# Performance work log

Measured on AMD Instinct MI355X. Metric: run time of the kernel, lower is better.

The kernel has to match this reference:

```python
import jax, jax.numpy as jnp
import numpy as np

EPS = 1e-5

def _layernorm(x, w, b):
    mu = jnp.mean(x, axis=-1, keepdims=True)
    var = jnp.mean(jnp.square(x - mu), axis=-1, keepdims=True)
    return (x - mu) * jax.lax.rsqrt(var + EPS) * w + b

def setup_inputs() -> dict:
    key = jax.random.key(0)
    ks = jax.random.split(key, 9)
    N, P_DIM, D = 16384, 3072, 1024
    patches = jax.random.normal(ks[0], (N, P_DIM), dtype=jnp.float32)
    bbox_coords = jax.random.uniform(ks[1], (N, 4), dtype=jnp.float32)
    ln1_w = jnp.ones((P_DIM,), dtype=jnp.float32)
    ln1_b = jnp.zeros((P_DIM,), dtype=jnp.float32)
    W_patch = jax.random.normal(ks[2], (D, P_DIM), dtype=jnp.float32) * (P_DIM ** -0.5)
    class_emb = jax.random.normal(ks[3], (1, 1, D), dtype=jnp.float32)
    W_pos = jax.random.normal(ks[4], (D, 4), dtype=jnp.float32) * 0.5
    b_pos = jax.random.normal(ks[5], (D,), dtype=jnp.float32) * 0.02
    class_pos = jax.random.normal(ks[6], (1, D), dtype=jnp.float32)
    return {"patches": patches, "bbox_coords": bbox_coords, "ln1_w": ln1_w,
            "ln1_b": ln1_b, "W_patch": W_patch, "class_emb": class_emb,
            "W_pos": W_pos, "b_pos": b_pos, "class_pos": class_pos}

def reference(patches, bbox_coords, ln1_w, ln1_b, W_patch, class_emb, W_pos, b_pos, class_pos):
    # Batched equivalent of the per-patch loop: LayerNorm -> Linear (no bias).
    # NOTE: torch code computes patch_norm2 but appends the PRE-norm2 embedding,
    # so norm2 is dead code and omitted here.
    x = _layernorm(patches, ln1_w, ln1_b)                      # [N, patch_dim]
    patch_embeds = jnp.einsum('np,dp->nd', x, W_patch)          # [N, D]
    embeddings = jnp.concatenate([class_emb, patch_embeds[None]], axis=1)  # [1, N+1, D]
    pos = jnp.einsum('nc,dc->nd', bbox_coords, W_pos) + b_pos   # [N, D]
    pos_full = jnp.concatenate([class_pos[None], pos[None]], axis=1)       # [1, N+1, D]
    return embeddings + pos_full
```

## Files before the change

### kernel.cpp

```cpp
#include <hip/hip_runtime.h>

typedef unsigned short u16;
typedef __attribute__((ext_vector_type(8))) short bf16x8;
typedef __attribute__((ext_vector_type(16))) float f32x16;

#define AS1C(p) ((const __attribute__((address_space(1))) void*)(p))
#define AS3(p)  ((__attribute__((address_space(3))) void*)(p))

#define CFENCE() asm volatile("" ::: "memory")

__device__ __forceinline__ u16 f2bf(float f) {
    unsigned u = __float_as_uint(f);
    u += 0x7fffu + ((u >> 16) & 1u);
    return (u16)(u >> 16);
}

__global__ __launch_bounds__(256) void prep_kernel(
    const float* __restrict__ x, const float* __restrict__ w,
    const float* __restrict__ b, const float* __restrict__ Wp,
    const float* __restrict__ ce, const float* __restrict__ cp,
    u16* __restrict__ A, u16* __restrict__ Wb, float* __restrict__ out,
    int N, int D, int K)
{
    const int blk = blockIdx.x;
    const int t = threadIdx.x;

    if (blk < N) {
        const float* xr = x + (size_t)blk * K;
        float4 v[3];
#pragma unroll
        for (int i = 0; i < 3; ++i)
            v[i] = *(const float4*)&xr[(i * 256 + t) * 4];

        float s = 0.f;
#pragma unroll
        for (int i = 0; i < 3; ++i) s += v[i].x + v[i].y + v[i].z + v[i].w;
#pragma unroll
        for (int off = 32; off; off >>= 1) s += __shfl_down(s, off);

        __shared__ float red[8];
        const int wid = t >> 6, lane = t & 63;
        if (lane == 0) red[wid] = s;
        __syncthreads();
        const float mu = (red[0] + red[1] + red[2] + red[3]) * (1.0f / 3072.0f);

        float sq = 0.f;
#pragma unroll
        for (int i = 0; i < 3; ++i) {
            float dx = v[i].x - mu, dy = v[i].y - mu, dz = v[i].z - mu, dw = v[i].w - mu;
            sq += dx * dx + dy * dy + dz * dz + dw * dw;
        }
#pragma unroll
        for (int off = 32; off; off >>= 1) sq += __shfl_down(sq, off);
        if (lane == 0) red[4 + wid] = sq;
        __syncthreads();
        const float var = (red[4] + red[5] + red[6] + red[7]) * (1.0f / 3072.0f);
        const float inv = rsqrtf(var + 1e-5f);

#pragma unroll
        for (int i = 0; i < 3; ++i) {
            const int j = (i * 256 + t) * 4;
            const float4 wv = *(const float4*)&w[j];
            const float4 bv = *(const float4*)&b[j];
            ushort4 o;
            o.x = f2bf((v[i].x - mu) * inv * wv.x + bv.x);
            o.y = f2bf((v[i].y - mu) * inv * wv.y + bv.y);
            o.z = f2bf((v[i].z - mu) * inv * wv.z + bv.z);
            o.w = f2bf((v[i].w - mu) * inv * wv.w + bv.w);
            *(ushort4*)&A[(size_t)blk * K + j] = o;
        }
    } else if (blk < N + D) {
        const int row = blk - N;
        const float* wr = Wp + (size_t)row * K;
#pragma unroll
        for (int i = 0; i < 3; ++i) {
            const int j = (i * 256 + t) * 4;
            const float4 v = *(const float4*)&wr[j];
            ushort4 o;
            o.x = f2bf(v.x); o.y = f2bf(v.y); o.z = f2bf(v.z); o.w = f2bf(v.w);
            *(ushort4*)&Wb[(size_t)row * K + j] = o;
        }
    } else {
#pragma unroll
        for (int i = 0; i < 4; ++i) {
            const int j = i * 256 + t;
            out[j] = ce[j] + cp[j];
        }
    }
}

#define STG_A(BUFOFS, R0, T_) \
    __builtin_amdgcn_global_load_lds(AS1C(aS + (size_t)(R0) * 3072 + (T_) * 64), \
                                     AS3(dA + (BUFOFS) + (R0) * 128), 16, 0, 0)
#define STG_B(BUFOFS, R0, T_) \
    __builtin_amdgcn_global_load_lds(AS1C(bS + (size_t)(R0) * 3072 + (T_) * 64), \
                                     AS3(dB + (BUFOFS) + (R0) * 128), 16, 0, 0)

#define MFMA32(d, a, b) d = __builtin_amdgcn_mfma_f32_32x32x16_bf16(a, b, d, 0, 0, 0)

#define LGKM(N_) asm volatile("s_waitcnt lgkmcnt(" #N_ ")" ::: "memory"); \
                 __builtin_amdgcn_sched_barrier(0)

#define PH32(BUF, CK, STG, WT) do {                                               \
    const char* Ab = L + (BUF) + aRowBase;                                        \
    const char* Bb = L + (BUF) + bRowBase;                                        \
    bf16x8 a0 = *(const bf16x8*)(Ab + 0 * 4096 + (CK));                           \
    bf16x8 a1 = *(const bf16x8*)(Ab + 1 * 4096 + (CK));                           \
    bf16x8 b0 = *(const bf16x8*)(Bb + 0 * 4096 + (CK));                           \
    bf16x8 b1 = *(const bf16x8*)(Bb + 1 * 4096 + (CK));                           \
    bf16x8 a2 = *(const bf16x8*)(Ab + 2 * 4096 + (CK));                           \
    bf16x8 a3 = *(const bf16x8*)(Ab + 3 * 4096 + (CK));                           \
    STG;                                                                          \
    __builtin_amdgcn_s_setprio(1);                                                \
    LGKM(2);                                                                      \
    MFMA32(acc[0][0], a0, b0); MFMA32(acc[1][0], a1, b0);                         \
    MFMA32(acc[0][1], a0, b1); MFMA32(acc[1][1], a1, b1);                         \
    LGKM(0);                                                                      \
    MFMA32(acc[2][0], a2, b0); MFMA32(acc[3][0], a3, b0);                         \
    MFMA32(acc[2][1], a2, b1); MFMA32(acc[3][1], a3, b1);                         \
    __builtin_amdgcn_s_setprio(0);                                                \
    WT;                                                                           \
    __builtin_amdgcn_s_barrier();                                                 \
    CFENCE();                                                                     \
} while (0)

__global__ __launch_bounds__(512, 2) void gemm_256_r13_kernel(
    const u16* __restrict__ A, const u16* __restrict__ W,
    const float* __restrict__ bbox, const float* __restrict__ Wpos,
    const float* __restrict__ bpos, float* __restrict__ out,
    int D)
{
    __shared__ __align__(16) char lds[131072];
    const char* L = (const char*)lds;
    const int K = 3072;
    const int NK = 48;

    const int bid = blockIdx.x;
    const int swb = (bid & 7) * 32 + (bid >> 3);
    const int bx = swb & 3;
    const int by = swb >> 2;
    const int brow = by * 256;
    const int bcol = bx * 256;

    const int t = threadIdx.x;
    const int wid = t >> 6, lane = t & 63;
    const int wm = wid >> 2;
    const int wn = wid & 3;
    const int l31 = lane & 31;
    const int klane16 = (lane >> 5) * 16;
    const int xorb = (lane & 7) << 4;
    const int aRowBase = (wm * 128 + l31) * 128;
    const int bRowBase = 32768 + (wn * 64 + l31) * 128;
    const int ck0 = (0  + klane16) ^ xorb;
    const int ck1 = (32 + klane16) ^ xorb;
    const int ck2 = (64 + klane16) ^ xorb;
    const int ck3 = (96 + klane16) ^ xorb;

    const int srow = t >> 3;
    const int scol = ((t & 7) ^ ((t >> 3) & 7)) * 8;
    const u16* aS = A + (size_t)(brow + srow) * K + scol;
    const u16* bS = W + (size_t)(bcol + srow) * K + scol;
    char* dA = (char*)lds + t * 16;
    char* dB = (char*)lds + 32768 + t * 16;

    f32x16 acc[4][2] = {};

    STG_B(0, 0, 0);   STG_B(0, 64, 0);  STG_B(0, 128, 0); STG_B(0, 192, 0);
    STG_A(0, 0, 0);   STG_A(0, 128, 0); STG_A(0, 64, 0);  STG_A(0, 192, 0);
    asm volatile("s_waitcnt vmcnt(0)" ::: "memory");
    __builtin_amdgcn_s_barrier();
    CFENCE();

    for (int T = 0; T < NK; T += 2) {
        const bool more = (T + 2) < NK;
        PH32(0, ck0, { STG_B(65536, 0, T + 1); STG_B(65536, 64, T + 1);
                       STG_B(65536, 128, T + 1); }, ((void)0));
        PH32(0, ck1, { STG_B(65536, 192, T + 1); STG_A(65536, 0, T + 1);
                       STG_A(65536, 128, T + 1); }, ((void)0));
        PH32(0, ck2, { STG_A(65536, 64, T + 1); STG_A(65536, 192, T + 1); }, ((void)0));
        PH32(0, ck3, ((void)0),
             { asm volatile("s_waitcnt vmcnt(0)" ::: "memory"); });
        PH32(65536, ck0, { if (more) { STG_B(0, 0, T + 2); STG_B(0, 64, T + 2);
                                       STG_B(0, 128, T + 2); } }, ((void)0));
        PH32(65536, ck1, { if (more) { STG_B(0, 192, T + 2); STG_A(0, 0, T + 2);
                                       STG_A(0, 128, T + 2); } }, ((void)0));
        PH32(65536, ck2, { if (more) { STG_A(0, 64, T + 2); STG_A(0, 192, T + 2); } }, ((void)0));
        PH32(65536, ck3, ((void)0),
             { if (more) asm volatile("s_waitcnt vmcnt(0)" ::: "memory"); });
    }

    float* Lf = (float*)lds;
    const int lrofs = (lane >> 5) * 4;
    const int cg = bcol + lane * 4;

    float4 wpv[4];
    float bpv[4];
#pragma unroll
    for (int j = 0; j < 4; ++j) {
        wpv[j] = *(const float4*)&Wpos[(cg + j) * 4];
        bpv[j] = bpos[cg + j];
    }

#pragma unroll
    for (int mb = 0; mb < 4; ++mb) {
        __builtin_amdgcn_s_barrier();
        CFENCE();
#pragma unroll
        for (int nb = 0; nb < 2; ++nb) {
            const int cc = wn * 64 + nb * 32 + l31;
#pragma unroll
            for (int reg = 0; reg < 16; ++reg) {
                const int frow = (reg & 3) + 8 * (reg >> 2) + lrofs;
                Lf[(wm * 32 + frow) * 256 + cc] = acc[mb][nb][reg];
            }
        }
        __builtin_amdgcn_s_barrier();
        CFENCE();
#pragma unroll
        for (int i = 0; i < 8; ++i) {
            const int lrow = wid + 8 * i;
            const int gr = brow + (lrow >> 5) * 128 + mb * 32 + (lrow & 31);
            const float4 v = *(const float4*)&Lf[lrow * 256 + lane * 4];
            const float4 bb = *(const float4*)&bbox[(size_t)gr * 4];
            float4 o;
            o.x = v.x + bpv[0] + bb.x * wpv[0].x + bb.y * wpv[0].y + bb.z * wpv[0].z + bb.w * wpv[0].w;
            o.y = v.y + bpv[1] + bb.x * wpv[1].x + bb.y * wpv[1].y + bb.z * wpv[1].z + bb.w * wpv[1].w;
            o.z = v.z + bpv[2] + bb.x * wpv[2].x + bb.y * wpv[2].y + bb.z * wpv[2].z + bb.w * wpv[2].w;
            o.w = v.w + bpv[3] + bb.x * wpv[3].x + bb.y * wpv[3].y + bb.z * wpv[3].z + bb.w * wpv[3].w;
            *(float4*)&out[(size_t)(gr + 1) * D + cg] = o;
        }
    }
}

extern "C" void kernel_launch(void* const* d_in, const int* in_sizes, int n_in,
                              void* d_out, int out_size, void* d_ws, size_t ws_size,
                              hipStream_t stream)
{
    const float* patches   = (const float*)d_in[0];
    const float* bbox      = (const float*)d_in[1];
    const float* ln1_w     = (const float*)d_in[2];
    const float* ln1_b     = (const float*)d_in[3];
    const float* W_patch   = (const float*)d_in[4];
    const float* class_emb = (const float*)d_in[5];
    const float* W_pos     = (const float*)d_in[6];
    const float* b_pos     = (const float*)d_in[7];
    const float* class_pos = (const float*)d_in[8];
    float* out = (float*)d_out;

    const int N = in_sizes[1] / 4;
    const int K = in_sizes[2];
    const int D = in_sizes[7];

    u16* Abf = (u16*)d_ws;
    u16* Wbf = Abf + (size_t)N * K;

    prep_kernel<<<N + D + 1, 256, 0, stream>>>(patches, ln1_w, ln1_b, W_patch,
                                               class_emb, class_pos, Abf, Wbf, out,
                                               N, D, K);

    const int nblk = (N / 256) * (D / 256);
    gemm_256_r13_kernel<<<nblk, 512, 0, stream>>>(Abf, Wbf, bbox, W_pos, b_pos, out, D);
}
```

Before: 157.8 us.

## Replace per-phase barriers with one barrier per K-tile and double-buffered register reads

The GEMM main loop used to run four phases per 64-wide K tile, each ending in a workgroup barrier and reading LDS fragments just before its MFMAs. It now processes the whole K tile in one block: two register sets (x/y) hold fragments for alternating k-chunks, so LDS reads for the next chunk are issued while the current chunk's MFMAs run, with graded lgkmcnt waits. All global-to-LDS prefetches for the next tile are issued at once at the start of the tile, and there is only one barrier per tile. This cuts barrier overhead and hides LDS latency, at the cost of more live vector registers under the 512-thread, 2-block launch bound, which could cause spills or lower occupancy.

```diff
diff --git a/kernel.cpp b/kernel.cpp
--- a/kernel.cpp
+++ b/kernel.cpp
@@ -101,30 +101,52 @@
 #define LGKM(N_) asm volatile("s_waitcnt lgkmcnt(" #N_ ")" ::: "memory"); \
                  __builtin_amdgcn_sched_barrier(0)
 
-#define PH32(BUF, CK, STG, WT) do {                                               \
-    const char* Ab = L + (BUF) + aRowBase;                                        \
-    const char* Bb = L + (BUF) + bRowBase;                                        \
-    bf16x8 a0 = *(const bf16x8*)(Ab + 0 * 4096 + (CK));                           \
-    bf16x8 a1 = *(const bf16x8*)(Ab + 1 * 4096 + (CK));                           \
-    bf16x8 b0 = *(const bf16x8*)(Bb + 0 * 4096 + (CK));                           \
-    bf16x8 b1 = *(const bf16x8*)(Bb + 1 * 4096 + (CK));                           \
-    bf16x8 a2 = *(const bf16x8*)(Ab + 2 * 4096 + (CK));                           \
-    bf16x8 a3 = *(const bf16x8*)(Ab + 3 * 4096 + (CK));                           \
-    STG;                                                                          \
-    __builtin_amdgcn_s_setprio(1);                                                \
-    LGKM(2);                                                                      \
-    MFMA32(acc[0][0], a0, b0); MFMA32(acc[1][0], a1, b0);                         \
-    MFMA32(acc[0][1], a0, b1); MFMA32(acc[1][1], a1, b1);                         \
-    LGKM(0);                                                                      \
-    MFMA32(acc[2][0], a2, b0); MFMA32(acc[3][0], a3, b0);                         \
-    MFMA32(acc[2][1], a2, b1); MFMA32(acc[3][1], a3, b1);                         \
-    __builtin_amdgcn_s_setprio(0);                                                \
-    WT;                                                                           \
-    __builtin_amdgcn_s_barrier();                                                 \
-    CFENCE();                                                                     \
+#define RD6(BUF, CK, A0, A1, B0, B1, A2, A3) \
+    A0 = *(const bf16x8*)(L + (BUF) + aRowBase + 0 * 4096 + (CK)); \
+    A1 = *(const bf16x8*)(L + (BUF) + aRowBase + 1 * 4096 + (CK)); \
+    B0 = *(const bf16x8*)(L + (BUF) + bRowBase + 0 * 4096 + (CK)); \
+    B1 = *(const bf16x8*)(L + (BUF) + bRowBase + 1 * 4096 + (CK)); \
+    A2 = *(const bf16x8*)(L + (BUF) + aRowBase + 2 * 4096 + (CK)); \
+    A3 = *(const bf16x8*)(L + (BUF) + aRowBase + 3 * 4096 + (CK))
+
+#define G0(A0, A1, B0, B1) \
+    MFMA32(acc[0][0], A0, B0); MFMA32(acc[1][0], A1, B0); \
+    MFMA32(acc[0][1], A0, B1); MFMA32(acc[1][1], A1, B1)
+#define G1(A2, A3, B0, B1) \
+    MFMA32(acc[2][0], A2, B0); MFMA32(acc[3][0], A3, B0); \
+    MFMA32(acc[2][1], A2, B1); MFMA32(acc[3][1], A3, B1)
+
+#define TILE(BUF, STG, WT) do {                                                 \
+    bf16x8 xa0, xa1, xb0, xb1, xa2, xa3;                                        \
+    bf16x8 ya0, ya1, yb0, yb1, ya2, ya3;                                        \
+    RD6(BUF, ck0, xa0, xa1, xb0, xb1, xa2, xa3);                                \
+    RD6(BUF, ck1, ya0, ya1, yb0, yb1, ya2, ya3);                                \
+    STG;                                                                        \
+    __builtin_amdgcn_s_setprio(1);                                              \
+    LGKM(8); G0(xa0, xa1, xb0, xb1);                                            \
+    LGKM(6); G1(xa2, xa3, xb0, xb1);                                            \
+    RD6(BUF, ck2, xa0, xa1, xb0, xb1, xa2, xa3);                                \
+    LGKM(8); G0(ya0, ya1, yb0, yb1);                                            \
+    LGKM(6); G1(ya2, ya3, yb0, yb1);                                            \
+    RD6(BUF, ck3, ya0, ya1, yb0, yb1, ya2, ya3);                                \
+    LGKM(8); G0(xa0, xa1, xb0, xb1);                                            \
+    LGKM(6); G1(xa2, xa3, xb0, xb1);                                            \
+    LGKM(2); G0(ya0, ya1, yb0, yb1);                                            \
+    LGKM(0); G1(ya2, ya3, yb0, yb1);                                            \
+    __builtin_amdgcn_s_setprio(0);                                              \
+    WT;                                                                         \
+    __builtin_amdgcn_s_barrier();                                               \
+    CFENCE();                                                                   \
 } while (0)
 
-__global__ __launch_bounds__(512, 2) void gemm_256_r13_kernel(
+#define STG_ALL(OBUF, TN) \
+    { STG_B(OBUF, 0, TN); STG_B(OBUF, 64, TN); STG_B(OBUF, 128, TN);            \
+      STG_B(OBUF, 192, TN); STG_A(OBUF, 0, TN); STG_A(OBUF, 64, TN);            \
+      STG_A(OBUF, 128, TN); STG_A(OBUF, 192, TN); }
+
+#define VMW0() asm volatile("s_waitcnt vmcnt(0)" ::: "memory")
+
+__global__ __launch_bounds__(512, 2) void gemm_256_r14_kernel(
     const u16* __restrict__ A, const u16* __restrict__ W,
     const float* __restrict__ bbox, const float* __restrict__ Wpos,
     const float* __restrict__ bpos, float* __restrict__ out,
@@ -165,28 +187,15 @@
 
     f32x16 acc[4][2] = {};
 
-    STG_B(0, 0, 0);   STG_B(0, 64, 0);  STG_B(0, 128, 0); STG_B(0, 192, 0);
-    STG_A(0, 0, 0);   STG_A(0, 128, 0); STG_A(0, 64, 0);  STG_A(0, 192, 0);
-    asm volatile("s_waitcnt vmcnt(0)" ::: "memory");
+    STG_ALL(0, 0);
+    VMW0();
     __builtin_amdgcn_s_barrier();
     CFENCE();
 
     for (int T = 0; T < NK; T += 2) {
         const bool more = (T + 2) < NK;
-        PH32(0, ck0, { STG_B(65536, 0, T + 1); STG_B(65536, 64, T + 1);
-                       STG_B(65536, 128, T + 1); }, ((void)0));
-        PH32(0, ck1, { STG_B(65536, 192, T + 1); STG_A(65536, 0, T + 1);
-                       STG_A(65536, 128, T + 1); }, ((void)0));
-        PH32(0, ck2, { STG_A(65536, 64, T + 1); STG_A(65536, 192, T + 1); }, ((void)0));
-        PH32(0, ck3, ((void)0),
-             { asm volatile("s_waitcnt vmcnt(0)" ::: "memory"); });
-        PH32(65536, ck0, { if (more) { STG_B(0, 0, T + 2); STG_B(0, 64, T + 2);
-                                       STG_B(0, 128, T + 2); } }, ((void)0));
-        PH32(65536, ck1, { if (more) { STG_B(0, 192, T + 2); STG_A(0, 0, T + 2);
-                                       STG_A(0, 128, T + 2); } }, ((void)0));
-        PH32(65536, ck2, { if (more) { STG_A(0, 64, T + 2); STG_A(0, 192, T + 2); } }, ((void)0));
-        PH32(65536, ck3, ((void)0),
-             { if (more) asm volatile("s_waitcnt vmcnt(0)" ::: "memory"); });
+        TILE(0, STG_ALL(65536, T + 1), { VMW0(); });
+        TILE(65536, { if (more) STG_ALL(0, T + 2); }, { if (more) VMW0(); });
     }
 
     float* Lf = (float*)lds;
@@ -259,5 +268,5 @@
                                                N, D, K);
 
     const int nblk = (N / 256) * (D / 256);
-    gemm_256_r13_kernel<<<nblk, 512, 0, stream>>>(Abf, Wbf, bbox, W_pos, b_pos, out, D);
-}
+    gemm_256_r14_kernel<<<nblk, 512, 0, stream>>>(Abf, Wbf, bbox, W_pos, b_pos, out, D);
+}
```

Result: no change. 159.6 us (+1.1%).
